# Kernel tuning notes

Hardware: AMD Instinct MI355X
Metric: run time of the kernel (lower is better)

The kernel has to match this reference:

```python
import jax, jax.numpy as jnp
import numpy as np

DIM = 768
NUM_EXPERTS = 4
NUM_HEADS = 12
HEAD_DIM = DIM // NUM_HEADS
MLP_HID = 4 * DIM
FC1_OUT = MLP_HID + 3 * DIM   # 5376 (mlp hidden + qkv)
FC2_IN = MLP_HID + DIM        # 3840 (mlp hidden + attn out)
FC2_OUT = 2 * DIM             # 1536 (mlp out + attn proj out)
CAP_FACTOR = 0.5
LN_EPS = 1e-6


def setup_inputs() -> dict:
    key = jax.random.key(0)
    ks = jax.random.split(key, 4)
    B, N = 8, 1024
    return {
        "x": jax.random.normal(ks[0], (B, N, DIM), jnp.float32),
        "w_router": jax.random.normal(ks[1], (NUM_EXPERTS, DIM), jnp.float32) * 0.02,
        "gamma1": jnp.ones((DIM,), jnp.float32),
        "beta1": jnp.zeros((DIM,), jnp.float32),
        "w1": jax.random.normal(ks[2], (FC1_OUT, DIM), jnp.float32) * 0.02,
        "b1": jnp.zeros((FC1_OUT,), jnp.float32),
        "w2": jax.random.normal(ks[3], (FC2_OUT, FC2_IN), jnp.float32) * 0.02,
        "b2": jnp.zeros((FC2_OUT,), jnp.float32),
    }


def reference(x, w_router, gamma1, beta1, w1, b1, w2, b2):
    B, N, C = x.shape
    E = NUM_EXPERTS
    cap = int(CAP_FACTOR * N)
    # nested (MoNE) per-expert active dims: [96, 192, 384, 768] for E=4, C=768
    m = np.array([C // 2 ** (E - 1 - e) for e in range(E)])
    in_mask = (np.arange(C)[None, :] < m[:, None]).astype(np.float32)  # [E, C]
    in_mask = jnp.asarray(in_mask)
    out_mask = jnp.concatenate([in_mask, in_mask], axis=-1)  # [E, 2C] for fc2 chunks

    # ---- expert-choice router ----
    logits = jnp.einsum('bnc,ec->bne', x, w_router)          # [B, N, E]
    probs = jax.nn.softmax(logits, axis=-1)
    gate, idx = jax.lax.top_k(jnp.swapaxes(probs, 1, 2), cap)  # [B, E, cap]
    dispatch = jax.nn.one_hot(idx, N, dtype=x.dtype)           # [B, E, cap, N]
    combine = dispatch * gate[..., None]                       # [B, E, cap, N]

    # ---- norm1 ----
    mu = jnp.mean(x, -1, keepdims=True)
    var = jnp.var(x, -1, keepdims=True)
    y = (x - mu) * jax.lax.rsqrt(var + LN_EPS) * gamma1 + beta1

    # ---- experts_choose_masked_contract (fc1, nested input dims) ----
    xg = jnp.einsum('becn,bnd->becd', dispatch, y)             # gather [B,E,cap,C]
    xg = xg * in_mask[None, :, None, :]                        # nested expert slice
    h = jnp.einsum('becd,fd->becf', xg, w1) + b1               # [B,E,cap,FC1_OUT]
    h = jnp.einsum('becn,becf->bnf', dispatch, h)              # scatter [B,N,FC1_OUT]

    x_mlp, x_qkv = h[..., :MLP_HID], h[..., MLP_HID:]

    # ---- attention ----
    qkv = x_qkv.reshape(B, N, 3, NUM_HEADS, HEAD_DIM).transpose(2, 0, 3, 1, 4)
    q, k, v = qkv[0], qkv[1], qkv[2]                           # [B,H,N,hd]
    scale = HEAD_DIM ** -0.5
    attn = jax.nn.softmax(jnp.einsum('bhqd,bhkd->bhqk', q, k) * scale, axis=-1)
    x_attn = jnp.einsum('bhqk,bhkd->bhqd', attn, v)
    x_attn = x_attn.transpose(0, 2, 1, 3).reshape(B, N, C)

    # ---- mlp activation + concat ----
    x_mlp = jax.nn.gelu(x_mlp, approximate=False)
    y2 = jnp.concatenate([x_mlp, x_attn], axis=-1)             # [B,N,FC2_IN]

    # ---- experts_choose_masked_expand (fc2, nested output dims, combine-weighted) ----
    yg = jnp.einsum('becn,bnf->becf', dispatch, y2)            # gather [B,E,cap,FC2_IN]
    o = jnp.einsum('becf,of->beco', yg, w2) + b2               # [B,E,cap,FC2_OUT]
    o = o * out_mask[None, :, None, :]                         # nested expert output slice
    z = jnp.einsum('becn,beco->bno', combine, o)               # combine [B,N,FC2_OUT]

    x_mlp2, x_attn2 = z[..., :C], z[..., C:]
    return x + x_mlp2 + x_attn2
```

## Files before the change

kernel.cpp:

```cpp
#include <hip/hip_runtime.h>
#include <math.h>

typedef __bf16 bf16_t;
typedef __bf16 bf16x8 __attribute__((ext_vector_type(8)));
typedef __bf16 bf16x4 __attribute__((ext_vector_type(4)));
typedef float f32x4 __attribute__((ext_vector_type(4)));

#define DIM 768
#define NE 4
#define NH 12
#define HD 64
#define MLP_HID 3072
#define FC1_OUT 5376
#define FC2_IN 3840
#define CAP 512
#define LOG2E 1.44269504088896340736f

__device__ __forceinline__ void async_copy16(const void* g, void* l) {
  __builtin_amdgcn_global_load_lds((const __attribute__((address_space(1))) void*)g,
                                   (__attribute__((address_space(3))) void*)l, 16, 0, 0);
}

__device__ __forceinline__ float gelu_f(float v) {
  float v2 = v * v;
  float t = v * fmaf(-0.102944f, v2, -2.302208f);
  float e = exp2f(t);
  return v * __builtin_amdgcn_rcpf(1.0f + e);
}

__global__ __launch_bounds__(256) void cast_router_kernel(const float* __restrict__ w1,
                                                          const float* __restrict__ w2,
                                                          bf16_t* __restrict__ w1b,
                                                          bf16_t* __restrict__ w2b,
                                                          const float* __restrict__ x,
                                                          const float* __restrict__ wr,
                                                          float* __restrict__ probs) {
  if (blockIdx.x < 2048) {
    const int N1 = FC1_OUT * DIM;
    const int N2 = 1536 * FC2_IN;
    for (int i = blockIdx.x * 256 + threadIdx.x; i < N1 + N2; i += 2048 * 256) {
      if (i < N1) w1b[i] = (bf16_t)w1[i];
      else        w2b[i - N1] = (bf16_t)w2[i - N1];
    }
    return;
  }
  int t = (blockIdx.x - 2048) * 4 + (threadIdx.x >> 6);
  int l = threadIdx.x & 63;
  const float* xr = x + (size_t)t * DIM;
  float a0 = 0.f, a1 = 0.f, a2 = 0.f, a3 = 0.f;
#pragma unroll
  for (int i = 0; i < 12; i++) {
    int d = l + i * 64;
    float xv = xr[d];
    a0 += xv * wr[d];
    a1 += xv * wr[DIM + d];
    a2 += xv * wr[2 * DIM + d];
    a3 += xv * wr[3 * DIM + d];
  }
#pragma unroll
  for (int off = 32; off > 0; off >>= 1) {
    a0 += __shfl_down(a0, off);
    a1 += __shfl_down(a1, off);
    a2 += __shfl_down(a2, off);
    a3 += __shfl_down(a3, off);
  }
  if (l == 0) {
    float m = fmaxf(fmaxf(a0, a1), fmaxf(a2, a3));
    float e0 = expf(a0 - m), e1 = expf(a1 - m), e2 = expf(a2 - m), e3 = expf(a3 - m);
    float inv = 1.0f / (e0 + e1 + e2 + e3);
    int b = t >> 10, n = t & 1023;
    probs[(b * NE + 0) * 1024 + n] = e0 * inv;
    probs[(b * NE + 1) * 1024 + n] = e1 * inv;
    probs[(b * NE + 2) * 1024 + n] = e2 * inv;
    probs[(b * NE + 3) * 1024 + n] = e3 * inv;
  }
}

__global__ __launch_bounds__(256) void rank_kernel(const float* __restrict__ probs,
                                                   float* __restrict__ gate_tok) {
  int be = blockIdx.y;
  __shared__ float p[1024];
  for (int i = threadIdx.x; i < 1024; i += 256) p[i] = probs[be * 1024 + i];
  __syncthreads();
  int n = blockIdx.x * 256 + threadIdx.x;
  float pn = p[n];
  int rank = 0;
  for (int j = 0; j < 1024; j++) {
    float pj = p[j];
    rank += (pj > pn) || (pj == pn && j < n);
  }
  int b = be >> 2, e = be & 3;
  gate_tok[(size_t)((b << 10) + n) * 4 + e] = (rank < CAP) ? pn : 0.0f;
}

__global__ __launch_bounds__(256) void ln_kernel(const float* __restrict__ x,
                                                 const float* __restrict__ gamma,
                                                 const float* __restrict__ beta,
                                                 const float* __restrict__ gate_tok,
                                                 bf16_t* __restrict__ ytil,
                                                 float* __restrict__ cntf,
                                                 float* __restrict__ g4) {
  int t = blockIdx.x * 4 + (threadIdx.x >> 6);
  int l = threadIdx.x & 63;
  float4 gg = ((const float4*)gate_tok)[t];
  float s0 = (gg.x > 0.f) ? 1.f : 0.f;
  float s1 = (gg.y > 0.f) ? 1.f : 0.f;
  float s2 = (gg.z > 0.f) ? 1.f : 0.f;
  float s3 = (gg.w > 0.f) ? 1.f : 0.f;
  float c3 = s3, c2 = c3 + s2, c1 = c2 + s1, c0 = c1 + s0;
  if (l == 0) {
    cntf[t] = c0;
    float4 G;
    G.x = gg.x + gg.y + gg.z + gg.w;
    G.y = gg.y + gg.z + gg.w;
    G.z = gg.z + gg.w;
    G.w = gg.w;
    ((float4*)g4)[t] = G;
  }
  const float* xr = x + (size_t)t * DIM;
  float v[12];
  float s = 0.f, sq = 0.f;
#pragma unroll
  for (int i = 0; i < 12; i++) {
    v[i] = xr[l + i * 64];
    s += v[i];
    sq += v[i] * v[i];
  }
#pragma unroll
  for (int off = 1; off < 64; off <<= 1) {
    s += __shfl_xor(s, off);
    sq += __shfl_xor(sq, off);
  }
  float mean = s * (1.0f / DIM);
  float var = sq * (1.0f / DIM) - mean * mean;
  float rs = rsqrtf(var + 1e-6f);
#pragma unroll
  for (int i = 0; i < 12; i++) {
    int d = l + i * 64;
    float cf = (d < 96) ? c0 : (d < 192) ? c1 : (d < 384) ? c2 : c3;
    ytil[(size_t)t * DIM + d] = (bf16_t)(((v[i] - mean) * rs * gamma[d] + beta[d]) * cf);
  }
}

__global__ __launch_bounds__(256, 4) void fc1_kernel(const bf16_t* __restrict__ ytil,
                                                     const bf16_t* __restrict__ w1b,
                                                     const float* __restrict__ b1,
                                                     const float* __restrict__ cntf,
                                                     bf16_t* __restrict__ y2b,
                                                     bf16_t* __restrict__ qb,
                                                     bf16_t* __restrict__ kb,
                                                     bf16_t* __restrict__ vtb) {
  const int bid = blockIdx.x;
  const int xcd = bid & 7, j = bid >> 3;
  const int mt = xcd * 8 + (j & 7);
  const int nt = j >> 3;
  const int tid = threadIdx.x;
  const int w = tid >> 6, l = tid & 63;
  const int lq = l >> 4, lr = l & 15;

  __shared__ __align__(16) bf16_t lA[128 * 64];
  __shared__ __align__(16) bf16_t lB[128 * 64];

  f32x4 acc[4][4] = {};
  const int mwave = (w & 1) * 64, nwave = (w >> 1) * 64;
  const int crow = l >> 3;
  const int cbg = (l & 7) ^ (crow & 7);

  for (int k0 = 0; k0 < DIM; k0 += 64) {
#pragma unroll
    for (int i = 0; i < 4; i++) {
      int c = w * 4 + i;
      int row = c * 8 + crow;
      async_copy16(ytil + (size_t)(mt * 128 + row) * DIM + k0 + cbg * 8, lA + c * 512);
      async_copy16(w1b + (size_t)(nt * 128 + row) * DIM + k0 + cbg * 8, lB + c * 512);
    }
    __syncthreads();
#pragma unroll
    for (int ks = 0; ks < 2; ks++) {
      const int cbA = ((ks * 4 + lq) ^ (lr & 7)) * 8;
      bf16x8 af[4], bfr[4];
#pragma unroll
      for (int mi = 0; mi < 4; mi++)
        af[mi] = *(const bf16x8*)(lA + (mwave + mi * 16 + lr) * 64 + cbA);
#pragma unroll
      for (int ni = 0; ni < 4; ni++)
        bfr[ni] = *(const bf16x8*)(lB + (nwave + ni * 16 + lr) * 64 + cbA);
#pragma unroll
      for (int mi = 0; mi < 4; mi++)
#pragma unroll
        for (int ni = 0; ni < 4; ni++)
          acc[mi][ni] = __builtin_amdgcn_mfma_f32_16x16x32_bf16(af[mi], bfr[ni], acc[mi][ni], 0, 0, 0);
    }
    __syncthreads();
  }

#pragma unroll
  for (int mi = 0; mi < 4; mi++) {
    int row0 = mt * 128 + mwave + mi * 16 + lq * 4;
    float cnt[4];
#pragma unroll
    for (int r = 0; r < 4; r++) cnt[r] = cntf[row0 + r];
#pragma unroll
    for (int ni = 0; ni < 4; ni++) {
      int col = nt * 128 + nwave + ni * 16 + lr;
      float bias = b1[col];
      if (col < MLP_HID) {
#pragma unroll
        for (int r = 0; r < 4; r++) {
          float v = acc[mi][ni][r] + cnt[r] * bias;
          y2b[(size_t)(row0 + r) * FC2_IN + col] = (bf16_t)gelu_f(v);
        }
      } else {
        int part = col - MLP_HID;
        int comp = (part >= 1536) ? 2 : (part >= 768) ? 1 : 0;
        int rem = part - comp * 768;
        int hh = rem >> 6, d = rem & 63;
        int b = row0 >> 10, n0 = row0 & 1023;
        size_t base = (size_t)(b * NH + hh);
        if (comp == 2) {
          bf16x4 pk;
#pragma unroll
          for (int r = 0; r < 4; r++)
            pk[r] = (bf16_t)(acc[mi][ni][r] + cnt[r] * bias);
          *(bf16x4*)(vtb + (base * HD + d) * 1024 + n0) = pk;
        } else {
#pragma unroll
          for (int r = 0; r < 4; r++) {
            float v = acc[mi][ni][r] + cnt[r] * bias;
            if (comp == 0) qb[(base * 1024 + n0 + r) * HD + d] = (bf16_t)(v * (0.125f * LOG2E));
            else           kb[(base * 1024 + n0 + r) * HD + d] = (bf16_t)v;
          }
        }
      }
    }
  }
}

__global__ __launch_bounds__(256) void attn_kernel(const bf16_t* __restrict__ qb,
                                                   const bf16_t* __restrict__ kb,
                                                   const bf16_t* __restrict__ vtb,
                                                   bf16_t* __restrict__ y2b) {
  const int bid = blockIdx.x;
  const int xcd = bid & 7, j = bid >> 3;
  const int bh = xcd * 12 + (j >> 3);
  const int qt = j & 7;
  const int tid = threadIdx.x;
  const int w = tid >> 6, l = tid & 63, lq = l >> 4, lr = l & 15;

  __shared__ __align__(16) bf16_t lK[64 * 64];
  __shared__ __align__(16) bf16_t lV[64 * 64];
  __shared__ __align__(16) bf16_t lP[4][16 * 72];

  const bf16_t* qbase = qb + (size_t)bh * 1024 * HD;
  const bf16_t* kbase = kb + (size_t)bh * 1024 * HD;
  const bf16_t* vbase = vtb + (size_t)bh * HD * 1024;

  bf16x8 qf[2][2];
#pragma unroll
  for (int h = 0; h < 2; h++) {
    int qrow = qt * 128 + h * 64 + w * 16 + lr;
#pragma unroll
    for (int s = 0; s < 2; s++)
      qf[h][s] = *(const bf16x8*)(qbase + (size_t)qrow * HD + s * 32 + lq * 8);
  }

  f32x4 oacc[2][4] = {};
  float psum[2][4] = {};

  const int crow = l >> 3;
  const int cbg = (l & 7) ^ (crow & 7);

  for (int kt = 0; kt < 16; kt++) {
#pragma unroll
    for (int i = 0; i < 2; i++) {
      int c = w * 2 + i;
      int row = c * 8 + crow;
      async_copy16(kbase + (size_t)(kt * 64 + row) * HD + cbg * 8, lK + c * 512);
      async_copy16(vbase + (size_t)row * 1024 + kt * 64 + cbg * 8, lV + c * 512);
    }
    __syncthreads();

#pragma unroll
    for (int h = 0; h < 2; h++) {
      f32x4 sacc[4] = {};
#pragma unroll
      for (int s = 0; s < 2; s++) {
        const int cb = ((s * 4 + lq) ^ (lr & 7)) * 8;
#pragma unroll
        for (int kbq = 0; kbq < 4; kbq++) {
          bf16x8 kf = *(const bf16x8*)(lK + (kbq * 16 + lr) * 64 + cb);
          sacc[kbq] = __builtin_amdgcn_mfma_f32_16x16x32_bf16(qf[h][s], kf, sacc[kbq], 0, 0, 0);
        }
      }

#pragma unroll
      for (int kbq = 0; kbq < 4; kbq++)
#pragma unroll
        for (int r = 0; r < 4; r++) {
          float pv = exp2f(sacc[kbq][r]);
          psum[h][r] += pv;
          lP[w][(lq * 4 + r) * 72 + kbq * 16 + lr] = (bf16_t)pv;
        }

      bf16x8 pf[2];
#pragma unroll
      for (int s = 0; s < 2; s++)
        pf[s] = *(const bf16x8*)(&lP[w][lr * 72 + s * 32 + lq * 8]);

#pragma unroll
      for (int s = 0; s < 2; s++) {
        const int cb = ((s * 4 + lq) ^ (lr & 7)) * 8;
#pragma unroll
        for (int nb = 0; nb < 4; nb++) {
          bf16x8 vf = *(const bf16x8*)(lV + (nb * 16 + lr) * 64 + cb);
          oacc[h][nb] = __builtin_amdgcn_mfma_f32_16x16x32_bf16(pf[s], vf, oacc[h][nb], 0, 0, 0);
        }
      }
    }
    __syncthreads();
  }

  int b = bh / NH, hh = bh % NH;
#pragma unroll
  for (int h = 0; h < 2; h++) {
#pragma unroll
    for (int off = 1; off < 16; off <<= 1)
#pragma unroll
      for (int r = 0; r < 4; r++) psum[h][r] += __shfl_xor(psum[h][r], off);
    float rinv[4];
#pragma unroll
    for (int r = 0; r < 4; r++) rinv[r] = 1.0f / psum[h][r];
#pragma unroll
    for (int nb = 0; nb < 4; nb++)
#pragma unroll
      for (int r = 0; r < 4; r++) {
        float v = oacc[h][nb][r] * rinv[r];
        int tok = qt * 128 + h * 64 + w * 16 + lq * 4 + r;
        y2b[((size_t)(b * 1024 + tok)) * FC2_IN + MLP_HID + hh * HD + nb * 16 + lr] = (bf16_t)v;
      }
  }
}

__global__ __launch_bounds__(256, 4) void fc2_kernel(const bf16_t* __restrict__ y2b,
                                                     const bf16_t* __restrict__ w2b,
                                                     const float* __restrict__ b2,
                                                     const float* __restrict__ g4,
                                                     const float* __restrict__ x,
                                                     float* __restrict__ out) {
  const int bid = blockIdx.x;
  const int xcd = bid & 7, j = bid >> 3;
  const int mt = xcd * 8 + j / 12;
  const int ct = j % 12;
  const int tid = threadIdx.x;
  const int w = tid >> 6, l = tid & 63;
  const int lq = l >> 4, lr = l & 15;

  __shared__ __align__(16) bf16_t lA[128 * 64];
  __shared__ __align__(16) bf16_t lB[128 * 64];

  f32x4 acc[2][4][2] = {};
  const int mwave = (w & 1) * 64, nwave = (w >> 1) * 32;
  const int crow = l >> 3;
  const int cbg = (l & 7) ^ (crow & 7);

  for (int k0 = 0; k0 < FC2_IN; k0 += 64) {
#pragma unroll
    for (int i = 0; i < 4; i++) {
      int c = w * 4 + i;
      int row = c * 8 + crow;
      async_copy16(y2b + (size_t)(mt * 128 + row) * FC2_IN + k0 + cbg * 8, lA + c * 512);
      int grow = ((row >> 6) * 768) + ct * 64 + (row & 63);
      async_copy16(w2b + (size_t)grow * FC2_IN + k0 + cbg * 8, lB + c * 512);
    }
    __syncthreads();
#pragma unroll
    for (int ks = 0; ks < 2; ks++) {
      const int cbA = ((ks * 4 + lq) ^ (lr & 7)) * 8;
      bf16x8 af[4], bfr[2][2];
#pragma unroll
      for (int mi = 0; mi < 4; mi++)
        af[mi] = *(const bf16x8*)(lA + (mwave + mi * 16 + lr) * 64 + cbA);
#pragma unroll
      for (int h = 0; h < 2; h++)
#pragma unroll
        for (int ni = 0; ni < 2; ni++)
          bfr[h][ni] = *(const bf16x8*)(lB + (h * 64 + nwave + ni * 16 + lr) * 64 + cbA);
#pragma unroll
      for (int h = 0; h < 2; h++)
#pragma unroll
        for (int mi = 0; mi < 4; mi++)
#pragma unroll
          for (int ni = 0; ni < 2; ni++)
            acc[h][mi][ni] = __builtin_amdgcn_mfma_f32_16x16x32_bf16(af[mi], bfr[h][ni], acc[h][mi][ni], 0, 0, 0);
    }
    __syncthreads();
  }

#pragma unroll
  for (int mi = 0; mi < 4; mi++) {
    int row0 = mt * 128 + mwave + mi * 16 + lq * 4;
    float4 G[4];
#pragma unroll
    for (int r = 0; r < 4; r++) G[r] = ((const float4*)g4)[row0 + r];
#pragma unroll
    for (int ni = 0; ni < 2; ni++) {
      int col = ct * 64 + nwave + ni * 16 + lr;
      float b20 = b2[col], b21 = b2[768 + col];
#pragma unroll
      for (int r = 0; r < 4; r++) {
        float gw = (col < 96) ? G[r].x : (col < 192) ? G[r].y : (col < 384) ? G[r].z : G[r].w;
        float o = (acc[0][mi][ni][r] + b20) + (acc[1][mi][ni][r] + b21);
        size_t idx = (size_t)(row0 + r) * DIM + col;
        out[idx] = x[idx] + gw * o;
      }
    }
  }
}

extern "C" void kernel_launch(void* const* d_in, const int* in_sizes, int n_in,
                              void* d_out, int out_size, void* d_ws, size_t ws_size,
                              hipStream_t stream) {
  const float* x     = (const float*)d_in[0];
  const float* wr    = (const float*)d_in[1];
  const float* gamma = (const float*)d_in[2];
  const float* beta  = (const float*)d_in[3];
  const float* w1    = (const float*)d_in[4];
  const float* b1    = (const float*)d_in[5];
  const float* w2    = (const float*)d_in[6];
  const float* b2    = (const float*)d_in[7];
  float* out = (float*)d_out;

  char* ws = (char*)d_ws;
  float*  probs    = (float*)(ws + 0);
  float*  gate_tok = (float*)(ws + 131072);
  float*  cntf     = (float*)(ws + 262144);
  float*  g4       = (float*)(ws + 294912);
  bf16_t* w1b      = (bf16_t*)(ws + 425984);
  bf16_t* w2b      = (bf16_t*)(ws + 8683520);
  bf16_t* ytil     = (bf16_t*)(ws + 20480000);
  bf16_t* y2b      = (bf16_t*)(ws + 33062912);
  bf16_t* qb       = (bf16_t*)(ws + 95977472);
  bf16_t* kb       = (bf16_t*)(ws + 108560384);
  bf16_t* vtb      = (bf16_t*)(ws + 121143296);

  cast_router_kernel<<<4096, 256, 0, stream>>>(w1, w2, w1b, w2b, x, wr, probs);
  rank_kernel<<<dim3(4, 32), 256, 0, stream>>>(probs, gate_tok);
  ln_kernel<<<2048, 256, 0, stream>>>(x, gamma, beta, gate_tok, ytil, cntf, g4);
  fc1_kernel<<<2688, 256, 0, stream>>>(ytil, w1b, b1, cntf, y2b, qb, kb, vtb);
  attn_kernel<<<768, 256, 0, stream>>>(qb, kb, vtb, y2b);
  fc2_kernel<<<768, 256, 0, stream>>>(y2b, w2b, b2, g4, x, out);
}
```

Before: 368.0 us.

## Enlarge fc2 tiles to 256x192 with double-buffered async LDS pipeline

The fc2 GEMM now uses 512-thread blocks computing 256-row by 192-column tiles, where the two halves (mlp and attn) are interleaved per row so each wave can sum them with a lane shuffle. LDS is double-buffered, with manual waitcnt and barriers so the next k-tile loads while the current one computes, and s_setprio is raised during MFMA. This aims to improve data reuse per load and hide global-load latency. The cost is fewer blocks (256), higher register and LDS use, and half the lanes idle during the epilogue store.

```diff
diff --git a/kernel.cpp b/kernel.cpp
--- a/kernel.cpp
+++ b/kernel.cpp
@@ -341,7 +341,7 @@
   }
 }
 
-__global__ __launch_bounds__(256, 4) void fc2_kernel(const bf16_t* __restrict__ y2b,
+__global__ __launch_bounds__(512, 2) void fc2_kernel(const bf16_t* __restrict__ y2b,
                                                      const bf16_t* __restrict__ w2b,
                                                      const float* __restrict__ b2,
                                                      const float* __restrict__ g4,
@@ -349,69 +349,104 @@
                                                      float* __restrict__ out) {
   const int bid = blockIdx.x;
   const int xcd = bid & 7, j = bid >> 3;
-  const int mt = xcd * 8 + j / 12;
-  const int ct = j % 12;
+  const int mt = xcd * 4 + (j >> 3);
+  const int ct = j & 7;
   const int tid = threadIdx.x;
   const int w = tid >> 6, l = tid & 63;
   const int lq = l >> 4, lr = l & 15;
-
-  __shared__ __align__(16) bf16_t lA[128 * 64];
-  __shared__ __align__(16) bf16_t lB[128 * 64];
-
-  f32x4 acc[2][4][2] = {};
-  const int mwave = (w & 1) * 64, nwave = (w >> 1) * 32;
+  const int wm = w & 1, wn = w >> 1;
+
+  __shared__ __align__(16) bf16_t lA[2][256 * 64];
+  __shared__ __align__(16) bf16_t lB[2][192 * 64];
+
+  f32x4 acc[8][3] = {};
   const int crow = l >> 3;
   const int cbg = (l & 7) ^ (crow & 7);
 
-  for (int k0 = 0; k0 < FC2_IN; k0 += 64) {
+  auto stage = [&](int buf, int k0) {
 #pragma unroll
     for (int i = 0; i < 4; i++) {
       int c = w * 4 + i;
       int row = c * 8 + crow;
-      async_copy16(y2b + (size_t)(mt * 128 + row) * FC2_IN + k0 + cbg * 8, lA + c * 512);
-      int grow = ((row >> 6) * 768) + ct * 64 + (row & 63);
-      async_copy16(w2b + (size_t)grow * FC2_IN + k0 + cbg * 8, lB + c * 512);
-    }
-    __syncthreads();
+      async_copy16(y2b + (size_t)(mt * 256 + row) * FC2_IN + k0 + cbg * 8, &lA[buf][c * 512]);
+    }
+#pragma unroll
+    for (int i = 0; i < 3; i++) {
+      int c = w * 3 + i;
+      int r = c * 8 + crow;
+      int grow = (r & 1) * 768 + ct * 96 + (r >> 1);
+      async_copy16(w2b + (size_t)grow * FC2_IN + k0 + cbg * 8, &lB[buf][c * 512]);
+    }
+  };
+
+  auto compute = [&](int buf) {
+    const bf16_t* la = lA[buf];
+    const bf16_t* lb = lB[buf];
+    __builtin_amdgcn_s_setprio(1);
 #pragma unroll
     for (int ks = 0; ks < 2; ks++) {
-      const int cbA = ((ks * 4 + lq) ^ (lr & 7)) * 8;
-      bf16x8 af[4], bfr[2][2];
-#pragma unroll
-      for (int mi = 0; mi < 4; mi++)
-        af[mi] = *(const bf16x8*)(lA + (mwave + mi * 16 + lr) * 64 + cbA);
-#pragma unroll
-      for (int h = 0; h < 2; h++)
-#pragma unroll
-        for (int ni = 0; ni < 2; ni++)
-          bfr[h][ni] = *(const bf16x8*)(lB + (h * 64 + nwave + ni * 16 + lr) * 64 + cbA);
-#pragma unroll
-      for (int h = 0; h < 2; h++)
-#pragma unroll
-        for (int mi = 0; mi < 4; mi++)
-#pragma unroll
-          for (int ni = 0; ni < 2; ni++)
-            acc[h][mi][ni] = __builtin_amdgcn_mfma_f32_16x16x32_bf16(af[mi], bfr[h][ni], acc[h][mi][ni], 0, 0, 0);
-    }
-    __syncthreads();
-  }
-
-#pragma unroll
-  for (int mi = 0; mi < 4; mi++) {
-    int row0 = mt * 128 + mwave + mi * 16 + lq * 4;
+      const int cb = ((ks * 4 + lq) ^ (lr & 7)) * 8;
+      bf16x8 af[8], bfr[3];
+#pragma unroll
+      for (int mi = 0; mi < 8; mi++)
+        af[mi] = *(const bf16x8*)(la + (wm * 128 + mi * 16 + lr) * 64 + cb);
+#pragma unroll
+      for (int ni = 0; ni < 3; ni++)
+        bfr[ni] = *(const bf16x8*)(lb + (wn * 48 + ni * 16 + lr) * 64 + cb);
+#pragma unroll
+      for (int mi = 0; mi < 8; mi++)
+#pragma unroll
+        for (int ni = 0; ni < 3; ni++)
+          acc[mi][ni] = __builtin_amdgcn_mfma_f32_16x16x32_bf16(af[mi], bfr[ni], acc[mi][ni], 0, 0, 0);
+    }
+    __builtin_amdgcn_s_setprio(0);
+  };
+
+  stage(0, 0);
+  stage(1, 64);
+  asm volatile("s_waitcnt vmcnt(7)" ::: "memory");
+  __builtin_amdgcn_s_barrier();
+  __builtin_amdgcn_sched_barrier(0);
+
+  int cur = 0;
+  for (int kt = 0; kt < 58; ++kt) {
+    compute(cur);
+    asm volatile("s_waitcnt lgkmcnt(0)" ::: "memory");
+    __builtin_amdgcn_sched_barrier(0);
+    __builtin_amdgcn_s_barrier();
+    __builtin_amdgcn_sched_barrier(0);
+    stage(cur, (kt + 2) * 64);
+    asm volatile("s_waitcnt vmcnt(7)" ::: "memory");
+    __builtin_amdgcn_s_barrier();
+    __builtin_amdgcn_sched_barrier(0);
+    cur ^= 1;
+  }
+  compute(cur);
+  asm volatile("s_waitcnt vmcnt(0)" ::: "memory");
+  __builtin_amdgcn_s_barrier();
+  __builtin_amdgcn_sched_barrier(0);
+  compute(cur ^ 1);
+
+  const int row_base = mt * 256 + wm * 128;
+#pragma unroll
+  for (int mi = 0; mi < 8; mi++) {
+    const int row0 = row_base + mi * 16 + lq * 4;
     float4 G[4];
 #pragma unroll
     for (int r = 0; r < 4; r++) G[r] = ((const float4*)g4)[row0 + r];
 #pragma unroll
-    for (int ni = 0; ni < 2; ni++) {
-      int col = ct * 64 + nwave + ni * 16 + lr;
-      float b20 = b2[col], b21 = b2[768 + col];
+    for (int ni = 0; ni < 3; ni++) {
+      const int col = ct * 96 + wn * 24 + ni * 8 + (lr >> 1);
+      const float bh = b2[(lr & 1) * 768 + col];
 #pragma unroll
       for (int r = 0; r < 4; r++) {
-        float gw = (col < 96) ? G[r].x : (col < 192) ? G[r].y : (col < 384) ? G[r].z : G[r].w;
-        float o = (acc[0][mi][ni][r] + b20) + (acc[1][mi][ni][r] + b21);
-        size_t idx = (size_t)(row0 + r) * DIM + col;
-        out[idx] = x[idx] + gw * o;
+        float s = acc[mi][ni][r] + bh;
+        s += __shfl_xor(s, 1);
+        if (!(lr & 1)) {
+          float gw = (col < 96) ? G[r].x : (col < 192) ? G[r].y : (col < 384) ? G[r].z : G[r].w;
+          size_t idx = (size_t)(row0 + r) * DIM + col;
+          out[idx] = x[idx] + gw * s;
+        }
       }
     }
   }
@@ -448,5 +483,5 @@
   ln_kernel<<<2048, 256, 0, stream>>>(x, gamma, beta, gate_tok, ytil, cntf, g4);
   fc1_kernel<<<2688, 256, 0, stream>>>(ytil, w1b, b1, cntf, y2b, qb, kb, vtb);
   attn_kernel<<<768, 256, 0, stream>>>(qb, kb, vtb, y2b);
-  fc2_kernel<<<768, 256, 0, stream>>>(y2b, w2b, b2, g4, x, out);
-}
+  fc2_kernel<<<256, 512, 0, stream>>>(y2b, w2b, b2, g4, x, out);
+}
```

Result: slower. 394.9 us (+7.3%).
